# Kernel optimization log

Measured on AMD Instinct MI355X. Metric: run time of the kernel, lower is better.

The kernel has to match this reference:

```python
import jax, jax.numpy as jnp
import numpy as np

EPS = 1e-8  # torch.cosine_similarity eps


def _unit(v):
    # normalize over last dim with per-vector eps clamp (torch cosine_similarity semantics)
    n = jnp.sqrt(jnp.sum(v * v, axis=-1, keepdims=True))
    return v / jnp.maximum(n, EPS)


def setup_inputs() -> dict:
    key = jax.random.key(0)
    ks = jax.random.split(key, 10)
    V, D, B, R, S, N, C = 100000, 300, 4096, 32, 32, 2, 2
    return {
        "tokens": jax.random.randint(ks[0], (B, R), 0, V),
        "support_idx": jax.random.randint(ks[1], (N, S), 0, V),
        "emb": jax.random.normal(ks[2], (V, D), jnp.float32) * 0.1,
        "conv1_w": jax.random.normal(ks[3], (2, 2, 3, 3), jnp.float32) * 0.1,
        "conv1_b": jnp.zeros((2,), jnp.float32),
        "conv2_w": jax.random.normal(ks[4], (2, 2, 2, 2), jnp.float32) * 0.1,
        "conv2_b": jnp.zeros((2,), jnp.float32),
        "fc2_w": jax.random.normal(ks[5], (2, 2), jnp.float32) * 0.5,
        "fc2_b": jnp.zeros((2,), jnp.float32),
        "fc_w": jax.random.normal(ks[6], (C, 128), jnp.float32) * 0.1,
        "fc_b": jnp.zeros((C,), jnp.float32),
    }


def reference(tokens, support_idx, emb, conv1_w, conv1_b, conv2_w, conv2_b,
              fc2_w, fc2_b, fc_w, fc_b):
    B = tokens.shape[0]
    # embedding lookups
    x = emb[tokens]          # [B, R, D]
    sv = emb[support_idx]    # [N, S, D]
    # fused normalize + batched matmul = cosine similarity matrix [B, N, S, R]
    sm = jnp.einsum('nsd,brd->bnsr', _unit(sv), _unit(x))
    # original detaches both operands of cosine_similarity
    sm = jax.lax.stop_gradient(sm)
    # channel bi-attention
    flat = sm.reshape(B, 2, -1)                       # [B, 2, S*R]
    attn = jax.nn.softmax(flat, axis=2)
    pooled = jnp.sum(attn * flat, axis=2)             # [B, 2]
    gate = jax.nn.sigmoid(pooled @ fc2_w.T + fc2_b)   # [B, 2]
    h = sm * gate[:, :, None, None]                   # [B, 2, S, R]
    # conv1 3x3 pad 1 + relu + maxpool 2x2
    dn = ('NCHW', 'OIHW', 'NCHW')
    h = jax.lax.conv_general_dilated(h, conv1_w, (1, 1), [(1, 1), (1, 1)],
                                     dimension_numbers=dn)
    h = jax.nn.relu(h + conv1_b[None, :, None, None])
    h = jax.lax.reduce_window(h, -jnp.inf, jax.lax.max,
                              (1, 1, 2, 2), (1, 1, 2, 2), 'VALID')
    # conv2 2x2 pad 1 + relu + avgpool 2x2
    h = jax.lax.conv_general_dilated(h, conv2_w, (1, 1), [(1, 1), (1, 1)],
                                     dimension_numbers=dn)
    h = jax.nn.relu(h + conv2_b[None, :, None, None])
    h = jax.lax.reduce_window(h, 0.0, jax.lax.add,
                              (1, 1, 2, 2), (1, 1, 2, 2), 'VALID') * 0.25
    # dropout is identity at inference; flatten -> [B, 128] -> fc
    h = h.reshape(B, -1)
    return h @ fc_w.T + fc_b
```

## Files before the change

kernel.cpp:

```cpp
#include <hip/hip_runtime.h>
#include <stdint.h>

#define DIM     300
#define NBATCH  4096
#define NSUP    64
#define KP      320
#define LSTR    328
#define SMST    82
#define SMY     36
#define GRID_G  256
#define PPB     16

typedef float f32x4 __attribute__((ext_vector_type(4)));
typedef short s16x8 __attribute__((ext_vector_type(8)));

static __device__ __forceinline__ unsigned bc(float x) { return __builtin_bit_cast(unsigned, x); }
static __device__ __forceinline__ float asf(unsigned u) { return __builtin_bit_cast(float, u); }
static __device__ __forceinline__ unsigned perm_hi(unsigned a, unsigned b) {
    return __builtin_amdgcn_perm(a, b, 0x07060302u);
}
static __device__ __forceinline__ unsigned short f2bf(float x) {
    unsigned u = bc(x);
    return (unsigned short)((u + 0x7FFFu + ((u >> 16) & 1u)) >> 16);
}
static __device__ __forceinline__ float bf2f(unsigned short h) { return asf((unsigned)h << 16); }

__global__ __launch_bounds__(64) void prep_kernel(
    const int* __restrict__ sidx, const float* __restrict__ emb,
    unsigned short* __restrict__ Bh, unsigned short* __restrict__ Bl) {
    const int j = blockIdx.x, l = threadIdx.x;
    const size_t tok = (size_t)sidx[j];
    const float* src = emb + tok * DIM;
    float e[5];
    #pragma unroll
    for (int c = 0; c < 5; ++c) {
        const int k = c * 64 + l;
        e[c] = (k < DIM) ? src[k] : 0.f;
    }
    float s = e[0]*e[0] + e[1]*e[1] + e[2]*e[2] + e[3]*e[3] + e[4]*e[4];
    #pragma unroll
    for (int m = 32; m >= 1; m >>= 1) s += __shfl_xor(s, m);
    const float rn = 1.f / fmaxf(sqrtf(s), 1e-8f);
    #pragma unroll
    for (int c = 0; c < 5; ++c) {
        const int k = c * 64 + l;
        const float v = (k < DIM) ? e[c] * rn : 0.f;
        const unsigned short h = f2bf(v);
        Bh[j * KP + k] = h;
        Bl[j * KP + k] = f2bf(v - bf2f(h));
    }
}

__global__ __launch_bounds__(512) void gemm_kernel(
    const int* __restrict__ tokens, const float* __restrict__ emb,
    const unsigned short* __restrict__ Bh, const unsigned short* __restrict__ Bl,
    float* __restrict__ smG) {

    __shared__ __attribute__((aligned(16))) unsigned short AhL[32 * LSTR];
    __shared__ __attribute__((aligned(16))) unsigned short AlL[32 * LSTR];
    __shared__ __attribute__((aligned(16))) unsigned short BhL[NSUP * LSTR];
    __shared__ __attribute__((aligned(16))) unsigned short BlL[NSUP * LSTR];
    __shared__ __attribute__((aligned(16))) float norms[32];

    const int tid = threadIdx.x;
    const int l = tid & 63;
    const int w = tid >> 6;
    const int c = l & 15, hq = l >> 4;
    const int rb = (w >> 2) * 16;
    const int cg = w & 3;
    const int chn = cg >> 1, sb = (cg & 1) * 16;
    const int bbase = blockIdx.x * PPB;

    #pragma unroll
    for (int m = 0; m < 10; ++m) {
        const int ci = tid + m * 512;
        const int plane = ci / 2560;
        const int rem = ci - plane * 2560;
        const int rr = rem / 40, jj = rem - rr * 40;
        const uint4 v = *(const uint4*)((plane ? Bl : Bh) + rr * KP + jj * 8);
        *(uint4*)((plane ? BlL : BhL) + rr * LSTR + jj * 8) = v;
    }
    if (tid < 448) {
        const int row = tid / 14, q = tid - 14 * row;
        ((unsigned*)AhL)[row * 164 + 150 + q] = 0u;
        ((unsigned*)AlL)[row * 164 + 150 + q] = 0u;
    }

    const int ci1 = tid + 512, ci2 = tid + 1024, ci3 = tid + 1536, ci4 = tid + 2048;
    const int r0 = tid / 75, j0 = tid - 75 * r0;
    const int r1 = ci1 / 75, j1 = ci1 - 75 * r1;
    const int r2 = ci2 / 75, j2 = ci2 - 75 * r2;
    const int r3 = ci3 / 75, j3 = ci3 - 75 * r3;
    const int r4 = ci4 / 75, j4 = ci4 - 75 * r4;
    const bool has4 = (ci4 < 2400);

    const int abase = (rb + c) * LSTR + hq * 8;
    const int bbl   = (cg * 16 + c) * LSTR + hq * 8;

    float4 st0, st1, st2, st3, st4;

    #define ISSUE_GATHER(TB)                                                        \
    {                                                                               \
        st0 = *(const float4*)(emb + (size_t)tokens[(TB) + r0] * DIM + j0 * 4);     \
        st1 = *(const float4*)(emb + (size_t)tokens[(TB) + r1] * DIM + j1 * 4);     \
        st2 = *(const float4*)(emb + (size_t)tokens[(TB) + r2] * DIM + j2 * 4);     \
        st3 = *(const float4*)(emb + (size_t)tokens[(TB) + r3] * DIM + j3 * 4);     \
        if (has4) st4 = *(const float4*)(emb + (size_t)tokens[(TB) + r4] * DIM + j4 * 4); \
    }

    #define STORE_CHUNK(ST, R, J)                                                   \
    {                                                                               \
        const unsigned u0 = bc(ST.x) + 0x8000u, u1 = bc(ST.y) + 0x8000u;            \
        const unsigned u2 = bc(ST.z) + 0x8000u, u3 = bc(ST.w) + 0x8000u;            \
        const float q0f = ST.x - asf(u0 & 0xffff0000u);                             \
        const float q1f = ST.y - asf(u1 & 0xffff0000u);                             \
        const float q2f = ST.z - asf(u2 & 0xffff0000u);                             \
        const float q3f = ST.w - asf(u3 & 0xffff0000u);                             \
        *(uint2*)(&AhL[(R) * LSTR + (J) * 4]) =                                     \
            uint2{perm_hi(u1, u0), perm_hi(u3, u2)};                                \
        *(uint2*)(&AlL[(R) * LSTR + (J) * 4]) =                                     \
            uint2{perm_hi(bc(q1f) + 0x8000u, bc(q0f) + 0x8000u),                    \
                  perm_hi(bc(q3f) + 0x8000u, bc(q2f) + 0x8000u)};                   \
    }

    ISSUE_GATHER(bbase * 32);
    STORE_CHUNK(st0, r0, j0); STORE_CHUNK(st1, r1, j1); STORE_CHUNK(st2, r2, j2);
    STORE_CHUNK(st3, r3, j3);
    if (has4) STORE_CHUNK(st4, r4, j4);
    __syncthreads();

    #pragma unroll 1
    for (int p = 0; p < PPB; ++p) {
        if (p + 1 < PPB) ISSUE_GATHER((bbase + p + 1) * 32);
        __builtin_amdgcn_sched_barrier(0);

        f32x4 q0 = {0,0,0,0}, q1 = {0,0,0,0}, q2 = {0,0,0,0};
        f32x4 gv = {0,0,0,0}, g2 = {0,0,0,0};
        #pragma unroll
        for (int t = 0; t < 10; ++t) {
            const s16x8 ah = *(const s16x8*)(AhL + abase + t * 32);
            const s16x8 al = *(const s16x8*)(AlL + abase + t * 32);
            const s16x8 bh = *(const s16x8*)(BhL + bbl + t * 32);
            const s16x8 bl = *(const s16x8*)(BlL + bbl + t * 32);
            q0 = __builtin_amdgcn_mfma_f32_16x16x32_bf16(ah, bh, q0, 0, 0, 0);
            q1 = __builtin_amdgcn_mfma_f32_16x16x32_bf16(ah, bl, q1, 0, 0, 0);
            q2 = __builtin_amdgcn_mfma_f32_16x16x32_bf16(al, bh, q2, 0, 0, 0);
            gv = __builtin_amdgcn_mfma_f32_16x16x32_bf16(ah, ah, gv, 0, 0, 0);
            g2 = __builtin_amdgcn_mfma_f32_16x16x32_bf16(ah, al, g2, 0, 0, 0);
        }

        if (hq == (c >> 2)) {
            const int q = c & 3;
            const float d1 = (q == 0) ? gv[0] : (q == 1) ? gv[1] : (q == 2) ? gv[2] : gv[3];
            const float d2 = (q == 0) ? g2[0] : (q == 1) ? g2[1] : (q == 2) ? g2[2] : g2[3];
            norms[rb + c] = d1 + 2.f * d2;
        }
        asm volatile("s_waitcnt lgkmcnt(0)" ::: "memory");
        const f32x4 n4 = *(const f32x4*)&norms[rb + hq * 4];
        float4 vv;
        #pragma unroll
        for (int q = 0; q < 4; ++q) {
            const float rn = __builtin_amdgcn_rcpf(
                fmaxf(__builtin_amdgcn_sqrtf(n4[q]), 1e-8f));
            ((float*)&vv)[q] = (q0[q] + q1[q] + q2[q]) * rn;
        }
        *(float4*)(smG + ((size_t)((bbase + p) * 2 + chn) * 32 + sb + c) * 32 + rb + hq * 4) = vv;

        __syncthreads();
        if (p + 1 < PPB) {
            STORE_CHUNK(st0, r0, j0); STORE_CHUNK(st1, r1, j1); STORE_CHUNK(st2, r2, j2);
            STORE_CHUNK(st3, r3, j3);
            if (has4) STORE_CHUNK(st4, r4, j4);
        }
        __syncthreads();
    }
    #undef STORE_CHUNK
    #undef ISSUE_GATHER
}

__global__ __launch_bounds__(256) void tail_kernel(
    const float* __restrict__ smG,
    const float* __restrict__ c1w, const float* __restrict__ c1b,
    const float* __restrict__ c2w, const float* __restrict__ c2b,
    const float* __restrict__ f2w, const float* __restrict__ f2b,
    const float* __restrict__ fcw, const float* __restrict__ fcb,
    float* __restrict__ out) {

    __shared__ __attribute__((aligned(16))) float smP[34 * SMST];
    __shared__ __attribute__((aligned(16))) float pl1P[2 * 17 * 18];
    __shared__ float scrP[8];

    const int tid = threadIdx.x;
    const int w = tid >> 6, l = tid & 63;
    const int b = blockIdx.x;

    {
        const f32x4 z = {0.f, 0.f, 0.f, 0.f};
        #pragma unroll
        for (int i = 0; i < 3; ++i) {
            const int idx = i * 256 + tid;
            if (idx < 697) ((f32x4*)smP)[idx] = z;
        }
        if (tid >= 190) {
            const int z2 = tid - 190;
            const int ic = (z2 >= 33) ? 1 : 0;
            const int rm = z2 - 33 * ic;
            pl1P[ic * 306 + (rm < 17 ? rm : (rm - 16) * 18)] = 0.f;
        }
    }
    __syncthreads();

    {
        const float* src = smG + (size_t)b * 2048;
        float se = 0.f, sv = 0.f;
        #pragma unroll
        for (int h2 = 0; h2 < 2; ++h2) {
            const int f4 = tid * 2 + h2;
            const float4 v = ((const float4*)src)[f4];
            const int base = f4 * 4;
            const int chn = base >> 10;
            const int s = (base >> 5) & 31;
            const int r = base & 31;
            float* dstp = &smP[(r + 1) * SMST + chn * SMY + (s + 1)];
            dstp[0] = v.x; dstp[SMST] = v.y; dstp[2 * SMST] = v.z; dstp[3 * SMST] = v.w;
            const float e0 = __expf(v.x), e1 = __expf(v.y);
            const float e2 = __expf(v.z), e3 = __expf(v.w);
            se += e0 + e1 + e2 + e3;
            sv = fmaf(e0, v.x, sv); sv = fmaf(e1, v.y, sv);
            sv = fmaf(e2, v.z, sv); sv = fmaf(e3, v.w, sv);
        }
        #pragma unroll
        for (int m = 32; m >= 1; m >>= 1) { se += __shfl_xor(se, m); sv += __shfl_xor(sv, m); }
        if (l == 0) { scrP[w] = se; scrP[4 + w] = sv; }
    }
    __syncthreads();

    {
        const int ii = tid >> 4, jj = tid & 15;
        float pc0[4] = {0,0,0,0}, pc1[4] = {0,0,0,0};
        float pA0[4] = {0,0,0,0}, pA1[4] = {0,0,0,0};
        #pragma unroll
        for (int ic = 0; ic < 2; ++ic) {
            float p[4][4];
            #pragma unroll
            for (int a = 0; a < 4; ++a) {
                const int off = (2 * jj + a) * SMST + ic * SMY + 2 * ii;
                const float2 v01 = *(const float2*)&smP[off];
                const float2 v23 = *(const float2*)&smP[off + 2];
                p[a][0] = v01.x; p[a][1] = v01.y; p[a][2] = v23.x; p[a][3] = v23.y;
            }
            #pragma unroll
            for (int py = 0; py < 2; ++py)
            #pragma unroll
            for (int px = 0; px < 2; ++px)
            #pragma unroll
            for (int dy = 0; dy < 3; ++dy)
            #pragma unroll
            for (int dx = 0; dx < 3; ++dx) {
                const float pv = p[px + dx][py + dy];
                const int pos = py * 2 + px;
                if (ic == 0) {
                    pc0[pos] = fmaf(c1w[0 * 9 + dy * 3 + dx], pv, pc0[pos]);
                    pc1[pos] = fmaf(c1w[2 * 9 + dy * 3 + dx], pv, pc1[pos]);
                } else {
                    pA0[pos] = fmaf(c1w[1 * 9 + dy * 3 + dx], pv, pA0[pos]);
                    pA1[pos] = fmaf(c1w[3 * 9 + dy * 3 + dx], pv, pA1[pos]);
                }
            }
        }
        const float p0 = (scrP[4] + scrP[5]) / (scrP[0] + scrP[1]);
        const float p1 = (scrP[6] + scrP[7]) / (scrP[2] + scrP[3]);
        const float gg0 = 1.f / (1.f + __expf(-(f2w[0] * p0 + f2w[1] * p1 + f2b[0])));
        const float gg1 = 1.f / (1.f + __expf(-(f2w[2] * p0 + f2w[3] * p1 + f2b[1])));
        const float b0 = c1b[0], b1 = c1b[1];
        float mx0 = 0.f, mx1 = 0.f;
        #pragma unroll
        for (int i = 0; i < 4; ++i) {
            mx0 = fmaxf(mx0, b0 + gg0 * pc0[i] + gg1 * pA0[i]);
            mx1 = fmaxf(mx1, b1 + gg0 * pc1[i] + gg1 * pA1[i]);
        }
        pl1P[0 * 306 + (ii + 1) * 18 + (jj + 1)] = mx0;
        pl1P[1 * 306 + (ii + 1) * 18 + (jj + 1)] = mx1;
    }
    __syncthreads();

    if (w == 0) {
        float o0 = 0.f, o1 = 0.f;
        #pragma unroll
        for (int h = 0; h < 2; ++h) {
            const int o = h * 64 + l, oc2 = o >> 6, ii2 = (o >> 3) & 7, jj2 = o & 7;
            float sum = 0.f;
            #pragma unroll
            for (int py = 0; py < 2; ++py)
            #pragma unroll
            for (int px = 0; px < 2; ++px) {
                const int y = 2 * ii2 + py, x = 2 * jj2 + px;
                float acc = c2b[oc2];
                #pragma unroll
                for (int ic = 0; ic < 2; ++ic)
                #pragma unroll
                for (int dy = 0; dy < 2; ++dy)
                #pragma unroll
                for (int dx = 0; dx < 2; ++dx)
                    acc += c2w[((oc2 * 2 + ic) * 2 + dy) * 2 + dx] *
                           pl1P[ic * 306 + (y + dy) * 18 + (x + dx)];
                sum += fmaxf(acc, 0.f);
            }
            const float val = 0.25f * sum;
            o0 = fmaf(val, fcw[o], o0);
            o1 = fmaf(val, fcw[128 + o], o1);
        }
        #pragma unroll
        for (int m = 32; m >= 1; m >>= 1) { o0 += __shfl_xor(o0, m); o1 += __shfl_xor(o1, m); }
        if (l == 0) {
            out[b * 2 + 0] = fcb[0] + o0;
            out[b * 2 + 1] = fcb[1] + o1;
        }
    }
}

extern "C" void kernel_launch(void* const* d_in, const int* in_sizes, int n_in,
                              void* d_out, int out_size, void* d_ws, size_t ws_size,
                              hipStream_t stream) {
    const int* tokens = (const int*)d_in[0];
    const int* sidx   = (const int*)d_in[1];
    const float* emb  = (const float*)d_in[2];
    const float* c1w  = (const float*)d_in[3];
    const float* c1b  = (const float*)d_in[4];
    const float* c2w  = (const float*)d_in[5];
    const float* c2b  = (const float*)d_in[6];
    const float* f2w  = (const float*)d_in[7];
    const float* f2b  = (const float*)d_in[8];
    const float* fcw  = (const float*)d_in[9];
    const float* fcb  = (const float*)d_in[10];

    float* smG = (float*)d_ws;
    unsigned short* Bh = (unsigned short*)((char*)d_ws + (size_t)NBATCH * 2048 * 4);
    unsigned short* Bl = Bh + NSUP * KP;

    prep_kernel<<<NSUP, 64, 0, stream>>>(sidx, emb, Bh, Bl);
    gemm_kernel<<<GRID_G, 512, 0, stream>>>(tokens, emb, Bh, Bl, smG);
    tail_kernel<<<NBATCH, 256, 0, stream>>>(smG, c1w, c1b, c2w, c2b,
                                            f2w, f2b, fcw, fcb, (float*)d_out);
}
```

Before: 69.03 us.

## Keep support fragments in registers and double-buffer token tiles in LDS

Each wave now loads its B (support-vector) hi/lo bf16 fragments once into registers instead of staging the whole B matrix in LDS and re-reading it every iteration. The A (token) staging buffers are double-buffered, so the next tile's embeddings are written to the alternate buffer before a single barrier, removing one __syncthreads per iteration. A launch-bounds hint of 2 blocks per CU is added. This cuts LDS traffic and footprint, but raises register pressure (20 extra 8-wide fragments), which risks spills under the tighter launch bound.

```diff
diff --git a/kernel.cpp b/kernel.cpp
--- a/kernel.cpp
+++ b/kernel.cpp
@@ -51,15 +51,13 @@
     }
 }
 
-__global__ __launch_bounds__(512) void gemm_kernel(
+__global__ __launch_bounds__(512, 2) void gemm_kernel(
     const int* __restrict__ tokens, const float* __restrict__ emb,
     const unsigned short* __restrict__ Bh, const unsigned short* __restrict__ Bl,
     float* __restrict__ smG) {
 
-    __shared__ __attribute__((aligned(16))) unsigned short AhL[32 * LSTR];
-    __shared__ __attribute__((aligned(16))) unsigned short AlL[32 * LSTR];
-    __shared__ __attribute__((aligned(16))) unsigned short BhL[NSUP * LSTR];
-    __shared__ __attribute__((aligned(16))) unsigned short BlL[NSUP * LSTR];
+    __shared__ __attribute__((aligned(16))) unsigned short AhL[2][32 * LSTR];
+    __shared__ __attribute__((aligned(16))) unsigned short AlL[2][32 * LSTR];
     __shared__ __attribute__((aligned(16))) float norms[32];
 
     const int tid = threadIdx.x;
@@ -71,19 +69,23 @@
     const int chn = cg >> 1, sb = (cg & 1) * 16;
     const int bbase = blockIdx.x * PPB;
 
-    #pragma unroll
-    for (int m = 0; m < 10; ++m) {
-        const int ci = tid + m * 512;
-        const int plane = ci / 2560;
-        const int rem = ci - plane * 2560;
-        const int rr = rem / 40, jj = rem - rr * 40;
-        const uint4 v = *(const uint4*)((plane ? Bl : Bh) + rr * KP + jj * 8);
-        *(uint4*)((plane ? BlL : BhL) + rr * LSTR + jj * 8) = v;
-    }
+    s16x8 rbh[10], rbl[10];
+    {
+        const unsigned short* pBh = Bh + (cg * 16 + c) * KP + hq * 8;
+        const unsigned short* pBl = Bl + (cg * 16 + c) * KP + hq * 8;
+        #pragma unroll
+        for (int t = 0; t < 10; ++t) {
+            rbh[t] = *(const s16x8*)(pBh + t * 32);
+            rbl[t] = *(const s16x8*)(pBl + t * 32);
+        }
+    }
+
     if (tid < 448) {
         const int row = tid / 14, q = tid - 14 * row;
-        ((unsigned*)AhL)[row * 164 + 150 + q] = 0u;
-        ((unsigned*)AlL)[row * 164 + 150 + q] = 0u;
+        ((unsigned*)AhL[0])[row * 164 + 150 + q] = 0u;
+        ((unsigned*)AlL[0])[row * 164 + 150 + q] = 0u;
+        ((unsigned*)AhL[1])[row * 164 + 150 + q] = 0u;
+        ((unsigned*)AlL[1])[row * 164 + 150 + q] = 0u;
     }
 
     const int ci1 = tid + 512, ci2 = tid + 1024, ci3 = tid + 1536, ci4 = tid + 2048;
@@ -95,7 +97,6 @@
     const bool has4 = (ci4 < 2400);
 
     const int abase = (rb + c) * LSTR + hq * 8;
-    const int bbl   = (cg * 16 + c) * LSTR + hq * 8;
 
     float4 st0, st1, st2, st3, st4;
 
@@ -108,7 +109,7 @@
         if (has4) st4 = *(const float4*)(emb + (size_t)tokens[(TB) + r4] * DIM + j4 * 4); \
     }
 
-    #define STORE_CHUNK(ST, R, J)                                                   \
+    #define STORE_CHUNK(AH, AL, ST, R, J)                                           \
     {                                                                               \
         const unsigned u0 = bc(ST.x) + 0x8000u, u1 = bc(ST.y) + 0x8000u;            \
         const unsigned u2 = bc(ST.z) + 0x8000u, u3 = bc(ST.w) + 0x8000u;            \
@@ -116,35 +117,41 @@
         const float q1f = ST.y - asf(u1 & 0xffff0000u);                             \
         const float q2f = ST.z - asf(u2 & 0xffff0000u);                             \
         const float q3f = ST.w - asf(u3 & 0xffff0000u);                             \
-        *(uint2*)(&AhL[(R) * LSTR + (J) * 4]) =                                     \
+        *(uint2*)(&(AH)[(R) * LSTR + (J) * 4]) =                                    \
             uint2{perm_hi(u1, u0), perm_hi(u3, u2)};                                \
-        *(uint2*)(&AlL[(R) * LSTR + (J) * 4]) =                                     \
+        *(uint2*)(&(AL)[(R) * LSTR + (J) * 4]) =                                    \
             uint2{perm_hi(bc(q1f) + 0x8000u, bc(q0f) + 0x8000u),                    \
                   perm_hi(bc(q3f) + 0x8000u, bc(q2f) + 0x8000u)};                   \
     }
 
+    #define STAGE_ALL(AH, AL)                                                       \
+    {                                                                               \
+        STORE_CHUNK(AH, AL, st0, r0, j0); STORE_CHUNK(AH, AL, st1, r1, j1);         \
+        STORE_CHUNK(AH, AL, st2, r2, j2); STORE_CHUNK(AH, AL, st3, r3, j3);         \
+        if (has4) STORE_CHUNK(AH, AL, st4, r4, j4);                                 \
+    }
+
     ISSUE_GATHER(bbase * 32);
-    STORE_CHUNK(st0, r0, j0); STORE_CHUNK(st1, r1, j1); STORE_CHUNK(st2, r2, j2);
-    STORE_CHUNK(st3, r3, j3);
-    if (has4) STORE_CHUNK(st4, r4, j4);
+    STAGE_ALL(AhL[0], AlL[0]);
     __syncthreads();
 
     #pragma unroll 1
     for (int p = 0; p < PPB; ++p) {
+        const int cur = p & 1, nxt = cur ^ 1;
         if (p + 1 < PPB) ISSUE_GATHER((bbase + p + 1) * 32);
         __builtin_amdgcn_sched_barrier(0);
 
+        const unsigned short* pAh = AhL[cur];
+        const unsigned short* pAl = AlL[cur];
         f32x4 q0 = {0,0,0,0}, q1 = {0,0,0,0}, q2 = {0,0,0,0};
         f32x4 gv = {0,0,0,0}, g2 = {0,0,0,0};
         #pragma unroll
         for (int t = 0; t < 10; ++t) {
-            const s16x8 ah = *(const s16x8*)(AhL + abase + t * 32);
-            const s16x8 al = *(const s16x8*)(AlL + abase + t * 32);
-            const s16x8 bh = *(const s16x8*)(BhL + bbl + t * 32);
-            const s16x8 bl = *(const s16x8*)(BlL + bbl + t * 32);
-            q0 = __builtin_amdgcn_mfma_f32_16x16x32_bf16(ah, bh, q0, 0, 0, 0);
-            q1 = __builtin_amdgcn_mfma_f32_16x16x32_bf16(ah, bl, q1, 0, 0, 0);
-            q2 = __builtin_amdgcn_mfma_f32_16x16x32_bf16(al, bh, q2, 0, 0, 0);
+            const s16x8 ah = *(const s16x8*)(pAh + abase + t * 32);
+            const s16x8 al = *(const s16x8*)(pAl + abase + t * 32);
+            q0 = __builtin_amdgcn_mfma_f32_16x16x32_bf16(ah, rbh[t], q0, 0, 0, 0);
+            q1 = __builtin_amdgcn_mfma_f32_16x16x32_bf16(ah, rbl[t], q1, 0, 0, 0);
+            q2 = __builtin_amdgcn_mfma_f32_16x16x32_bf16(al, rbh[t], q2, 0, 0, 0);
             gv = __builtin_amdgcn_mfma_f32_16x16x32_bf16(ah, ah, gv, 0, 0, 0);
             g2 = __builtin_amdgcn_mfma_f32_16x16x32_bf16(ah, al, g2, 0, 0, 0);
         }
@@ -166,14 +173,12 @@
         }
         *(float4*)(smG + ((size_t)((bbase + p) * 2 + chn) * 32 + sb + c) * 32 + rb + hq * 4) = vv;
 
+        if (p + 1 < PPB) {
+            STAGE_ALL(AhL[nxt], AlL[nxt]);
+        }
         __syncthreads();
-        if (p + 1 < PPB) {
-            STORE_CHUNK(st0, r0, j0); STORE_CHUNK(st1, r1, j1); STORE_CHUNK(st2, r2, j2);
-            STORE_CHUNK(st3, r3, j3);
-            if (has4) STORE_CHUNK(st4, r4, j4);
-        }
-        __syncthreads();
-    }
+    }
+    #undef STAGE_ALL
     #undef STORE_CHUNK
     #undef ISSUE_GATHER
 }
```

New measurement: 66.68 us. -3.4%, faster.

## Fuse tail attention/conv/fc stages into the GEMM kernel per batch item

Applied to the files above, without the earlier changes.

Moves the softmax-pool gate, conv1+maxpool, conv2+avgpool and fc stages into the GEMM kernel's per-batch loop. Each batch item's similarity tile now stays in shared memory instead of being written to a global workspace and read back by a second kernel. This removes a 32 MB round trip and one launch. In exchange it adds barriers and serial tail work inside the GEMM loop, and the 256-block grid limits how well the tail runs in parallel.

```diff
diff --git a/kernel.cpp b/kernel.cpp
--- a/kernel.cpp
+++ b/kernel.cpp
@@ -54,13 +54,21 @@
 __global__ __launch_bounds__(512) void gemm_kernel(
     const int* __restrict__ tokens, const float* __restrict__ emb,
     const unsigned short* __restrict__ Bh, const unsigned short* __restrict__ Bl,
-    float* __restrict__ smG) {
-
+    const float* __restrict__ c1w, const float* __restrict__ c1b,
+    const float* __restrict__ c2w, const float* __restrict__ c2b,
+    const float* __restrict__ f2w, const float* __restrict__ f2b,
+    const float* __restrict__ fcw, const float* __restrict__ fcb,
+    float* __restrict__ out) {
+
+    __shared__ __attribute__((aligned(16))) unsigned short BhL[NSUP * LSTR];
+    __shared__ __attribute__((aligned(16))) unsigned short BlL[NSUP * LSTR];
     __shared__ __attribute__((aligned(16))) unsigned short AhL[32 * LSTR];
     __shared__ __attribute__((aligned(16))) unsigned short AlL[32 * LSTR];
-    __shared__ __attribute__((aligned(16))) unsigned short BhL[NSUP * LSTR];
-    __shared__ __attribute__((aligned(16))) unsigned short BlL[NSUP * LSTR];
+    __shared__ __attribute__((aligned(16))) float smP[34 * SMST];
+    __shared__ __attribute__((aligned(16))) float pl1P[2 * 17 * 18];
     __shared__ __attribute__((aligned(16))) float norms[32];
+    __shared__ __attribute__((aligned(16))) float scrP[16];
+    __shared__ float scr2[4];
 
     const int tid = threadIdx.x;
     const int l = tid & 63;
@@ -68,22 +76,33 @@
     const int c = l & 15, hq = l >> 4;
     const int rb = (w >> 2) * 16;
     const int cg = w & 3;
-    const int chn = cg >> 1, sb = (cg & 1) * 16;
+    const int ch = cg >> 1, sb = (cg & 1) * 16;
     const int bbase = blockIdx.x * PPB;
+    const int oc = tid >> 8, ii = (tid >> 4) & 15, jj = tid & 15;
 
     #pragma unroll
     for (int m = 0; m < 10; ++m) {
         const int ci = tid + m * 512;
         const int plane = ci / 2560;
         const int rem = ci - plane * 2560;
-        const int rr = rem / 40, jj = rem - rr * 40;
-        const uint4 v = *(const uint4*)((plane ? Bl : Bh) + rr * KP + jj * 8);
-        *(uint4*)((plane ? BlL : BhL) + rr * LSTR + jj * 8) = v;
+        const int rr = rem / 40, jc = rem - rr * 40;
+        const uint4 v = *(const uint4*)((plane ? Bl : Bh) + rr * KP + jc * 8);
+        *(uint4*)((plane ? BlL : BhL) + rr * LSTR + jc * 8) = v;
     }
     if (tid < 448) {
         const int row = tid / 14, q = tid - 14 * row;
         ((unsigned*)AhL)[row * 164 + 150 + q] = 0u;
         ((unsigned*)AlL)[row * 164 + 150 + q] = 0u;
+    }
+    {
+        const f32x4 z = {0.f, 0.f, 0.f, 0.f};
+        ((f32x4*)smP)[tid] = z;
+        if (tid < 697 - 512) ((f32x4*)smP)[512 + tid] = z;
+    }
+    if (tid >= 446) {
+        const int z2 = tid - 446;
+        const int ic = z2 / 33, rm = z2 % 33;
+        pl1P[ic * 306 + (rm < 17 ? rm : (rm - 16) * 18)] = 0.f;
     }
 
     const int ci1 = tid + 512, ci2 = tid + 1024, ci3 = tid + 1536, ci4 = tid + 2048;
@@ -123,10 +142,15 @@
                   perm_hi(bc(q3f) + 0x8000u, bc(q2f) + 0x8000u)};                   \
     }
 
+    #define STAGE_ALL()                                                             \
+    {                                                                               \
+        STORE_CHUNK(st0, r0, j0); STORE_CHUNK(st1, r1, j1);                         \
+        STORE_CHUNK(st2, r2, j2); STORE_CHUNK(st3, r3, j3);                         \
+        if (has4) STORE_CHUNK(st4, r4, j4);                                         \
+    }
+
     ISSUE_GATHER(bbase * 32);
-    STORE_CHUNK(st0, r0, j0); STORE_CHUNK(st1, r1, j1); STORE_CHUNK(st2, r2, j2);
-    STORE_CHUNK(st3, r3, j3);
-    if (has4) STORE_CHUNK(st4, r4, j4);
+    STAGE_ALL();
     __syncthreads();
 
     #pragma unroll 1
@@ -157,138 +181,66 @@
         }
         asm volatile("s_waitcnt lgkmcnt(0)" ::: "memory");
         const f32x4 n4 = *(const f32x4*)&norms[rb + hq * 4];
-        float4 vv;
-        #pragma unroll
-        for (int q = 0; q < 4; ++q) {
-            const float rn = __builtin_amdgcn_rcpf(
-                fmaxf(__builtin_amdgcn_sqrtf(n4[q]), 1e-8f));
-            ((float*)&vv)[q] = (q0[q] + q1[q] + q2[q]) * rn;
-        }
-        *(float4*)(smG + ((size_t)((bbase + p) * 2 + chn) * 32 + sb + c) * 32 + rb + hq * 4) = vv;
-
+        {
+            const int s = sb + c;
+            float se = 0.f, sv = 0.f;
+            #pragma unroll
+            for (int q = 0; q < 4; ++q) {
+                const float rn = __builtin_amdgcn_rcpf(
+                    fmaxf(__builtin_amdgcn_sqrtf(n4[q]), 1e-8f));
+                const float v = (q0[q] + q1[q] + q2[q]) * rn;
+                smP[(rb + hq * 4 + q + 1) * SMST + ch * SMY + (s + 1)] = v;
+                const float e = __expf(v);
+                se += e; sv = fmaf(e, v, sv);
+            }
+            #pragma unroll
+            for (int m = 32; m >= 1; m >>= 1) { se += __shfl_xor(se, m); sv += __shfl_xor(sv, m); }
+            if (l == 0) { scrP[w] = se; scrP[8 + w] = sv; }
+        }
         __syncthreads();
-        if (p + 1 < PPB) {
-            STORE_CHUNK(st0, r0, j0); STORE_CHUNK(st1, r1, j1); STORE_CHUNK(st2, r2, j2);
-            STORE_CHUNK(st3, r3, j3);
-            if (has4) STORE_CHUNK(st4, r4, j4);
+
+        {
+            float pc[2][4] = {{0,0,0,0},{0,0,0,0}};
+            #pragma unroll
+            for (int ic = 0; ic < 2; ++ic) {
+                float pp[4][4];
+                #pragma unroll
+                for (int a = 0; a < 4; ++a) {
+                    const int off = (2 * jj + a) * SMST + ic * SMY + 2 * ii;
+                    const float2 v01 = *(const float2*)&smP[off];
+                    const float2 v23 = *(const float2*)&smP[off + 2];
+                    pp[a][0] = v01.x; pp[a][1] = v01.y; pp[a][2] = v23.x; pp[a][3] = v23.y;
+                }
+                #pragma unroll
+                for (int py = 0; py < 2; ++py)
+                #pragma unroll
+                for (int px = 0; px < 2; ++px)
+                #pragma unroll
+                for (int dy = 0; dy < 3; ++dy)
+                #pragma unroll
+                for (int dx = 0; dx < 3; ++dx)
+                    pc[ic][py * 2 + px] += c1w[(oc * 2 + ic) * 9 + dy * 3 + dx] *
+                                           pp[px + dx][py + dy];
+            }
+            const f32x4 s0 = *(const f32x4*)&scrP[0];
+            const f32x4 s1 = *(const f32x4*)&scrP[4];
+            const f32x4 s2 = *(const f32x4*)&scrP[8];
+            const f32x4 s3 = *(const f32x4*)&scrP[12];
+            const float p0 = (s2.x + s2.y + s3.x + s3.y) / (s0.x + s0.y + s1.x + s1.y);
+            const float p1 = (s2.z + s2.w + s3.z + s3.w) / (s0.z + s0.w + s1.z + s1.w);
+            const float gg0 = 1.f / (1.f + __expf(-(f2w[0] * p0 + f2w[1] * p1 + f2b[0])));
+            const float gg1 = 1.f / (1.f + __expf(-(f2w[2] * p0 + f2w[3] * p1 + f2b[1])));
+            const float bias = c1b[oc];
+            float mx = 0.f;
+            #pragma unroll
+            for (int i = 0; i < 4; ++i)
+                mx = fmaxf(mx, bias + gg0 * pc[0][i] + gg1 * pc[1][i]);
+            pl1P[oc * 306 + (ii + 1) * 18 + (jj + 1)] = mx;
         }
         __syncthreads();
-    }
-    #undef STORE_CHUNK
-    #undef ISSUE_GATHER
-}
-
-__global__ __launch_bounds__(256) void tail_kernel(
-    const float* __restrict__ smG,
-    const float* __restrict__ c1w, const float* __restrict__ c1b,
-    const float* __restrict__ c2w, const float* __restrict__ c2b,
-    const float* __restrict__ f2w, const float* __restrict__ f2b,
-    const float* __restrict__ fcw, const float* __restrict__ fcb,
-    float* __restrict__ out) {
-
-    __shared__ __attribute__((aligned(16))) float smP[34 * SMST];
-    __shared__ __attribute__((aligned(16))) float pl1P[2 * 17 * 18];
-    __shared__ float scrP[8];
-
-    const int tid = threadIdx.x;
-    const int w = tid >> 6, l = tid & 63;
-    const int b = blockIdx.x;
-
-    {
-        const f32x4 z = {0.f, 0.f, 0.f, 0.f};
-        #pragma unroll
-        for (int i = 0; i < 3; ++i) {
-            const int idx = i * 256 + tid;
-            if (idx < 697) ((f32x4*)smP)[idx] = z;
-        }
-        if (tid >= 190) {
-            const int z2 = tid - 190;
-            const int ic = (z2 >= 33) ? 1 : 0;
-            const int rm = z2 - 33 * ic;
-            pl1P[ic * 306 + (rm < 17 ? rm : (rm - 16) * 18)] = 0.f;
-        }
-    }
-    __syncthreads();
-
-    {
-        const float* src = smG + (size_t)b * 2048;
-        float se = 0.f, sv = 0.f;
-        #pragma unroll
-        for (int h2 = 0; h2 < 2; ++h2) {
-            const int f4 = tid * 2 + h2;
-            const float4 v = ((const float4*)src)[f4];
-            const int base = f4 * 4;
-            const int chn = base >> 10;
-            const int s = (base >> 5) & 31;
-            const int r = base & 31;
-            float* dstp = &smP[(r + 1) * SMST + chn * SMY + (s + 1)];
-            dstp[0] = v.x; dstp[SMST] = v.y; dstp[2 * SMST] = v.z; dstp[3 * SMST] = v.w;
-            const float e0 = __expf(v.x), e1 = __expf(v.y);
-            const float e2 = __expf(v.z), e3 = __expf(v.w);
-            se += e0 + e1 + e2 + e3;
-            sv = fmaf(e0, v.x, sv); sv = fmaf(e1, v.y, sv);
-            sv = fmaf(e2, v.z, sv); sv = fmaf(e3, v.w, sv);
-        }
-        #pragma unroll
-        for (int m = 32; m >= 1; m >>= 1) { se += __shfl_xor(se, m); sv += __shfl_xor(sv, m); }
-        if (l == 0) { scrP[w] = se; scrP[4 + w] = sv; }
-    }
-    __syncthreads();
-
-    {
-        const int ii = tid >> 4, jj = tid & 15;
-        float pc0[4] = {0,0,0,0}, pc1[4] = {0,0,0,0};
-        float pA0[4] = {0,0,0,0}, pA1[4] = {0,0,0,0};
-        #pragma unroll
-        for (int ic = 0; ic < 2; ++ic) {
-            float p[4][4];
-            #pragma unroll
-            for (int a = 0; a < 4; ++a) {
-                const int off = (2 * jj + a) * SMST + ic * SMY + 2 * ii;
-                const float2 v01 = *(const float2*)&smP[off];
-                const float2 v23 = *(const float2*)&smP[off + 2];
-                p[a][0] = v01.x; p[a][1] = v01.y; p[a][2] = v23.x; p[a][3] = v23.y;
-            }
-            #pragma unroll
-            for (int py = 0; py < 2; ++py)
-            #pragma unroll
-            for (int px = 0; px < 2; ++px)
-            #pragma unroll
-            for (int dy = 0; dy < 3; ++dy)
-            #pragma unroll
-            for (int dx = 0; dx < 3; ++dx) {
-                const float pv = p[px + dx][py + dy];
-                const int pos = py * 2 + px;
-                if (ic == 0) {
-                    pc0[pos] = fmaf(c1w[0 * 9 + dy * 3 + dx], pv, pc0[pos]);
-                    pc1[pos] = fmaf(c1w[2 * 9 + dy * 3 + dx], pv, pc1[pos]);
-                } else {
-                    pA0[pos] = fmaf(c1w[1 * 9 + dy * 3 + dx], pv, pA0[pos]);
-                    pA1[pos] = fmaf(c1w[3 * 9 + dy * 3 + dx], pv, pA1[pos]);
-                }
-            }
-        }
-        const float p0 = (scrP[4] + scrP[5]) / (scrP[0] + scrP[1]);
-        const float p1 = (scrP[6] + scrP[7]) / (scrP[2] + scrP[3]);
-        const float gg0 = 1.f / (1.f + __expf(-(f2w[0] * p0 + f2w[1] * p1 + f2b[0])));
-        const float gg1 = 1.f / (1.f + __expf(-(f2w[2] * p0 + f2w[3] * p1 + f2b[1])));
-        const float b0 = c1b[0], b1 = c1b[1];
-        float mx0 = 0.f, mx1 = 0.f;
-        #pragma unroll
-        for (int i = 0; i < 4; ++i) {
-            mx0 = fmaxf(mx0, b0 + gg0 * pc0[i] + gg1 * pA0[i]);
-            mx1 = fmaxf(mx1, b1 + gg0 * pc1[i] + gg1 * pA1[i]);
-        }
-        pl1P[0 * 306 + (ii + 1) * 18 + (jj + 1)] = mx0;
-        pl1P[1 * 306 + (ii + 1) * 18 + (jj + 1)] = mx1;
-    }
-    __syncthreads();
-
-    if (w == 0) {
-        float o0 = 0.f, o1 = 0.f;
-        #pragma unroll
-        for (int h = 0; h < 2; ++h) {
-            const int o = h * 64 + l, oc2 = o >> 6, ii2 = (o >> 3) & 7, jj2 = o & 7;
+
+        if (w < 2) {
+            const int oc2 = w, ii2 = l >> 3, jj2 = l & 7;
             float sum = 0.f;
             #pragma unroll
             for (int py = 0; py < 2; ++py)
@@ -307,16 +259,28 @@
                 sum += fmaxf(acc, 0.f);
             }
             const float val = 0.25f * sum;
-            o0 = fmaf(val, fcw[o], o0);
-            o1 = fmaf(val, fcw[128 + o], o1);
-        }
-        #pragma unroll
-        for (int m = 32; m >= 1; m >>= 1) { o0 += __shfl_xor(o0, m); o1 += __shfl_xor(o1, m); }
-        if (l == 0) {
-            out[b * 2 + 0] = fcb[0] + o0;
-            out[b * 2 + 1] = fcb[1] + o1;
-        }
-    }
+            const int o = w * 64 + l;
+            float t0 = val * fcw[o];
+            float t1 = val * fcw[128 + o];
+            #pragma unroll
+            for (int m = 32; m >= 1; m >>= 1) { t0 += __shfl_xor(t0, m); t1 += __shfl_xor(t1, m); }
+            if (l == 0) { scr2[w] = t0; scr2[2 + w] = t1; }
+        }
+        __syncthreads();
+
+        if (tid == 0) {
+            const int b = bbase + p;
+            out[b * 2 + 0] = fcb[0] + scr2[0] + scr2[1];
+            out[b * 2 + 1] = fcb[1] + scr2[2] + scr2[3];
+        }
+        if (p + 1 < PPB) {
+            STAGE_ALL();
+        }
+        __syncthreads();
+    }
+    #undef STAGE_ALL
+    #undef STORE_CHUNK
+    #undef ISSUE_GATHER
 }
 
 extern "C" void kernel_launch(void* const* d_in, const int* in_sizes, int n_in,
@@ -334,12 +298,11 @@
     const float* fcw  = (const float*)d_in[9];
     const float* fcb  = (const float*)d_in[10];
 
-    float* smG = (float*)d_ws;
-    unsigned short* Bh = (unsigned short*)((char*)d_ws + (size_t)NBATCH * 2048 * 4);
+    unsigned short* Bh = (unsigned short*)d_ws;
     unsigned short* Bl = Bh + NSUP * KP;
 
     prep_kernel<<<NSUP, 64, 0, stream>>>(sidx, emb, Bh, Bl);
-    gemm_kernel<<<GRID_G, 512, 0, stream>>>(tokens, emb, Bh, Bl, smG);
-    tail_kernel<<<NBATCH, 256, 0, stream>>>(smG, c1w, c1b, c2w, c2b,
+    gemm_kernel<<<GRID_G, 512, 0, stream>>>(tokens, emb, Bh, Bl,
+                                            c1w, c1b, c2w, c2b,
                                             f2w, f2b, fcw, fcb, (float*)d_out);
 }
```

Result: slower. 82.69 us (+19.8%).

## Double-buffer embedding gather registers to prefetch two panels ahead

Applied to the files above, without the earlier changes.

The gemm kernel now holds two register sets of gathered embedding rows and issues global loads two panels ahead, alternating A/B buffers in a loop unrolled by two. This lets global-memory latency for the token gather overlap with more MFMA work. It also adds a min-blocks-per-CU hint of 2 to launch_bounds and reorders the shared arrays. The extra live float4 registers raise register pressure and could cause spills under the tighter occupancy bound.

```diff
diff --git a/kernel.cpp b/kernel.cpp
--- a/kernel.cpp
+++ b/kernel.cpp
@@ -51,15 +51,15 @@
     }
 }
 
-__global__ __launch_bounds__(512) void gemm_kernel(
+__global__ __launch_bounds__(512, 2) void gemm_kernel(
     const int* __restrict__ tokens, const float* __restrict__ emb,
     const unsigned short* __restrict__ Bh, const unsigned short* __restrict__ Bl,
     float* __restrict__ smG) {
 
+    __shared__ __attribute__((aligned(16))) unsigned short BhL[NSUP * LSTR];
+    __shared__ __attribute__((aligned(16))) unsigned short BlL[NSUP * LSTR];
     __shared__ __attribute__((aligned(16))) unsigned short AhL[32 * LSTR];
     __shared__ __attribute__((aligned(16))) unsigned short AlL[32 * LSTR];
-    __shared__ __attribute__((aligned(16))) unsigned short BhL[NSUP * LSTR];
-    __shared__ __attribute__((aligned(16))) unsigned short BlL[NSUP * LSTR];
     __shared__ __attribute__((aligned(16))) float norms[32];
 
     const int tid = threadIdx.x;
@@ -76,9 +76,9 @@
         const int ci = tid + m * 512;
         const int plane = ci / 2560;
         const int rem = ci - plane * 2560;
-        const int rr = rem / 40, jj = rem - rr * 40;
-        const uint4 v = *(const uint4*)((plane ? Bl : Bh) + rr * KP + jj * 8);
-        *(uint4*)((plane ? BlL : BhL) + rr * LSTR + jj * 8) = v;
+        const int rr = rem / 40, jc = rem - rr * 40;
+        const uint4 v = *(const uint4*)((plane ? Bl : Bh) + rr * KP + jc * 8);
+        *(uint4*)((plane ? BlL : BhL) + rr * LSTR + jc * 8) = v;
     }
     if (tid < 448) {
         const int row = tid / 14, q = tid - 14 * row;
@@ -97,15 +97,16 @@
     const int abase = (rb + c) * LSTR + hq * 8;
     const int bbl   = (cg * 16 + c) * LSTR + hq * 8;
 
-    float4 st0, st1, st2, st3, st4;
-
-    #define ISSUE_GATHER(TB)                                                        \
+    float4 sA0, sA1, sA2, sA3, sA4;
+    float4 sB0, sB1, sB2, sB3, sB4;
+
+    #define ISSUE_GATHER(S0, S1, S2, S3, S4, TB)                                    \
     {                                                                               \
-        st0 = *(const float4*)(emb + (size_t)tokens[(TB) + r0] * DIM + j0 * 4);     \
-        st1 = *(const float4*)(emb + (size_t)tokens[(TB) + r1] * DIM + j1 * 4);     \
-        st2 = *(const float4*)(emb + (size_t)tokens[(TB) + r2] * DIM + j2 * 4);     \
-        st3 = *(const float4*)(emb + (size_t)tokens[(TB) + r3] * DIM + j3 * 4);     \
-        if (has4) st4 = *(const float4*)(emb + (size_t)tokens[(TB) + r4] * DIM + j4 * 4); \
+        S0 = *(const float4*)(emb + (size_t)tokens[(TB) + r0] * DIM + j0 * 4);      \
+        S1 = *(const float4*)(emb + (size_t)tokens[(TB) + r1] * DIM + j1 * 4);      \
+        S2 = *(const float4*)(emb + (size_t)tokens[(TB) + r2] * DIM + j2 * 4);      \
+        S3 = *(const float4*)(emb + (size_t)tokens[(TB) + r3] * DIM + j3 * 4);      \
+        if (has4) S4 = *(const float4*)(emb + (size_t)tokens[(TB) + r4] * DIM + j4 * 4); \
     }
 
     #define STORE_CHUNK(ST, R, J)                                                   \
@@ -123,57 +124,79 @@
                   perm_hi(bc(q3f) + 0x8000u, bc(q2f) + 0x8000u)};                   \
     }
 
-    ISSUE_GATHER(bbase * 32);
-    STORE_CHUNK(st0, r0, j0); STORE_CHUNK(st1, r1, j1); STORE_CHUNK(st2, r2, j2);
-    STORE_CHUNK(st3, r3, j3);
-    if (has4) STORE_CHUNK(st4, r4, j4);
+    #define STAGE_ALL(S0, S1, S2, S3, S4)                                           \
+    {                                                                               \
+        STORE_CHUNK(S0, r0, j0); STORE_CHUNK(S1, r1, j1);                           \
+        STORE_CHUNK(S2, r2, j2); STORE_CHUNK(S3, r3, j3);                           \
+        if (has4) STORE_CHUNK(S4, r4, j4);                                          \
+    }
+
+    #define COMPUTE_PANEL(PIDX)                                                     \
+    {                                                                               \
+        f32x4 q0 = {0,0,0,0}, q1 = {0,0,0,0}, q2 = {0,0,0,0};                       \
+        f32x4 gv = {0,0,0,0}, g2 = {0,0,0,0};                                       \
+        _Pragma("unroll")                                                           \
+        for (int t = 0; t < 10; ++t) {                                              \
+            const s16x8 ah = *(const s16x8*)(AhL + abase + t * 32);                 \
+            const s16x8 al = *(const s16x8*)(AlL + abase + t * 32);                 \
+            const s16x8 bh = *(const s16x8*)(BhL + bbl + t * 32);                   \
+            const s16x8 bl = *(const s16x8*)(BlL + bbl + t * 32);                   \
+            q0 = __builtin_amdgcn_mfma_f32_16x16x32_bf16(ah, bh, q0, 0, 0, 0);      \
+            q1 = __builtin_amdgcn_mfma_f32_16x16x32_bf16(ah, bl, q1, 0, 0, 0);      \
+            q2 = __builtin_amdgcn_mfma_f32_16x16x32_bf16(al, bh, q2, 0, 0, 0);      \
+            gv = __builtin_amdgcn_mfma_f32_16x16x32_bf16(ah, ah, gv, 0, 0, 0);      \
+            g2 = __builtin_amdgcn_mfma_f32_16x16x32_bf16(ah, al, g2, 0, 0, 0);      \
+        }                                                                           \
+        if (hq == (c >> 2)) {                                                       \
+            const int q = c & 3;                                                    \
+            const float d1 = (q == 0) ? gv[0] : (q == 1) ? gv[1]                    \
+                           : (q == 2) ? gv[2] : gv[3];                              \
+            const float d2 = (q == 0) ? g2[0] : (q == 1) ? g2[1]                    \
+                           : (q == 2) ? g2[2] : g2[3];                              \
+            norms[rb + c] = d1 + 2.f * d2;                                          \
+        }                                                                           \
+        asm volatile("s_waitcnt lgkmcnt(0)" ::: "memory");                          \
+        const f32x4 n4 = *(const f32x4*)&norms[rb + hq * 4];                        \
+        float4 vv;                                                                  \
+        _Pragma("unroll")                                                           \
+        for (int q = 0; q < 4; ++q) {                                               \
+            const float rn = __builtin_amdgcn_rcpf(                                 \
+                fmaxf(__builtin_amdgcn_sqrtf(n4[q]), 1e-8f));                       \
+            ((float*)&vv)[q] = (q0[q] + q1[q] + q2[q]) * rn;                        \
+        }                                                                           \
+        *(float4*)(smG + ((size_t)((PIDX) * 2 + chn) * 32 + sb + c) * 32            \
+                   + rb + hq * 4) = vv;                                             \
+    }
+
+    ISSUE_GATHER(sA0, sA1, sA2, sA3, sA4, bbase * 32);
+    STAGE_ALL(sA0, sA1, sA2, sA3, sA4);
+    ISSUE_GATHER(sA0, sA1, sA2, sA3, sA4, (bbase + 1) * 32);
+    ISSUE_GATHER(sB0, sB1, sB2, sB3, sB4, (bbase + 2) * 32);
+    __builtin_amdgcn_sched_barrier(0);
     __syncthreads();
 
     #pragma unroll 1
-    for (int p = 0; p < PPB; ++p) {
-        if (p + 1 < PPB) ISSUE_GATHER((bbase + p + 1) * 32);
+    for (int p = 0; p < PPB; p += 2) {
+        COMPUTE_PANEL(bbase + p);
+        __syncthreads();
+        STAGE_ALL(sA0, sA1, sA2, sA3, sA4);
+        if (p + 3 < PPB)
+            ISSUE_GATHER(sA0, sA1, sA2, sA3, sA4, (bbase + p + 3) * 32);
         __builtin_amdgcn_sched_barrier(0);
-
-        f32x4 q0 = {0,0,0,0}, q1 = {0,0,0,0}, q2 = {0,0,0,0};
-        f32x4 gv = {0,0,0,0}, g2 = {0,0,0,0};
-        #pragma unroll
-        for (int t = 0; t < 10; ++t) {
-            const s16x8 ah = *(const s16x8*)(AhL + abase + t * 32);
-            const s16x8 al = *(const s16x8*)(AlL + abase + t * 32);
-            const s16x8 bh = *(const s16x8*)(BhL + bbl + t * 32);
-            const s16x8 bl = *(const s16x8*)(BlL + bbl + t * 32);
-            q0 = __builtin_amdgcn_mfma_f32_16x16x32_bf16(ah, bh, q0, 0, 0, 0);
-            q1 = __builtin_amdgcn_mfma_f32_16x16x32_bf16(ah, bl, q1, 0, 0, 0);
-            q2 = __builtin_amdgcn_mfma_f32_16x16x32_bf16(al, bh, q2, 0, 0, 0);
-            gv = __builtin_amdgcn_mfma_f32_16x16x32_bf16(ah, ah, gv, 0, 0, 0);
-            g2 = __builtin_amdgcn_mfma_f32_16x16x32_bf16(ah, al, g2, 0, 0, 0);
-        }
-
-        if (hq == (c >> 2)) {
-            const int q = c & 3;
-            const float d1 = (q == 0) ? gv[0] : (q == 1) ? gv[1] : (q == 2) ? gv[2] : gv[3];
-            const float d2 = (q == 0) ? g2[0] : (q == 1) ? g2[1] : (q == 2) ? g2[2] : g2[3];
-            norms[rb + c] = d1 + 2.f * d2;
-        }
-        asm volatile("s_waitcnt lgkmcnt(0)" ::: "memory");
-        const f32x4 n4 = *(const f32x4*)&norms[rb + hq * 4];
-        float4 vv;
-        #pragma unroll
-        for (int q = 0; q < 4; ++q) {
-            const float rn = __builtin_amdgcn_rcpf(
-                fmaxf(__builtin_amdgcn_sqrtf(n4[q]), 1e-8f));
-            ((float*)&vv)[q] = (q0[q] + q1[q] + q2[q]) * rn;
-        }
-        *(float4*)(smG + ((size_t)((bbase + p) * 2 + chn) * 32 + sb + c) * 32 + rb + hq * 4) = vv;
-
         __syncthreads();
-        if (p + 1 < PPB) {
-            STORE_CHUNK(st0, r0, j0); STORE_CHUNK(st1, r1, j1); STORE_CHUNK(st2, r2, j2);
-            STORE_CHUNK(st3, r3, j3);
-            if (has4) STORE_CHUNK(st4, r4, j4);
-        }
+
+        COMPUTE_PANEL(bbase + p + 1);
         __syncthreads();
-    }
+        if (p + 2 < PPB) {
+            STAGE_ALL(sB0, sB1, sB2, sB3, sB4);
+            if (p + 4 < PPB)
+                ISSUE_GATHER(sB0, sB1, sB2, sB3, sB4, (bbase + p + 4) * 32);
+        }
+        __builtin_amdgcn_sched_barrier(0);
+        __syncthreads();
+    }
+    #undef COMPUTE_PANEL
+    #undef STAGE_ALL
     #undef STORE_CHUNK
     #undef ISSUE_GATHER
 }
```

Result: slower. 74.12 us (+7.4%).
